# Optimization experiments

Hardware: AMD Instinct MI355X
Metric: run time of the kernel (lower is better)

Reference implementation:

```python
import jax, jax.numpy as jnp
import numpy as np

TWO_N, D = 8192, 256
N = TWO_N // 2


def setup_inputs() -> dict:
    key = jax.random.key(0)
    k1, k2 = jax.random.split(key)
    embeddings = jax.random.normal(k1, (TWO_N, D), dtype=jnp.float32)
    pos_mask = jnp.zeros((N, TWO_N), dtype=bool)  # unused by the loss
    neg_mask = jax.random.randint(k2, (N, TWO_N), 0, 2).astype(bool)
    return {"embeddings": embeddings, "pos_mask": pos_mask, "neg_mask": neg_mask}


def reference(embeddings, pos_mask, neg_mask):
    # d[i, j] = <e_i, e_j>  (other_embeddings defaults to embeddings)
    d = jnp.matmul(embeddings, embeddings.T)            # [2N, 2N]
    n = embeddings.shape[0] // 2
    rows = d[:n]                                        # [N, 2N] (only rows 0..N-1 used)
    ap = rows[jnp.arange(n), jnp.arange(n) + n]         # d[i, i+N], shape [N]
    # masked sum_j exp(d[i,j] - ap_i) over negatives, then log(1 + .)
    expm = jnp.exp(rows - ap[:, None])                  # [N, 2N]
    j_all = jnp.log1p(jnp.sum(jnp.where(neg_mask, expm, 0.0), axis=1))  # [N]
    return jnp.mean(j_all)
```

## Files before the change

### kernel.cpp

```cpp
#include <hip/hip_runtime.h>
#include <math.h>

#define TWO_N 8192
#define NR 4096
#define D 256
#define PMW 128
#define L2E 1.44269504088896340736f

typedef __attribute__((ext_vector_type(8))) short bf16x8;
typedef __attribute__((ext_vector_type(4))) float f32x4;

#define AS1V const __attribute__((address_space(1))) void
#define AS3V __attribute__((address_space(3))) void
#define WAITVM(n) asm volatile("s_waitcnt vmcnt(" #n ")" ::: "memory")

__device__ inline unsigned short f2bf(float x) {
  unsigned u = __builtin_bit_cast(unsigned, x);
  u += 0x7fffu + ((u >> 16) & 1u);
  return (unsigned short)(u >> 16);
}

__global__ __launch_bounds__(256) void prep_kernel(
    const float* __restrict__ emb, const unsigned char* __restrict__ negm,
    unsigned short* __restrict__ ebf, unsigned long long* __restrict__ pm,
    float* __restrict__ apl, double* __restrict__ rowsum) {
  const int b = blockIdx.x, t = threadIdx.x;
  if (b < 1024) {
    const size_t i = ((size_t)b * 256 + t) * 8;
    const float4 a = *reinterpret_cast<const float4*>(emb + i);
    const float4 c = *reinterpret_cast<const float4*>(emb + i + 4);
    union { unsigned short s[8]; bf16x8 v; } o;
    o.s[0] = f2bf(a.x); o.s[1] = f2bf(a.y); o.s[2] = f2bf(a.z); o.s[3] = f2bf(a.w);
    o.s[4] = f2bf(c.x); o.s[5] = f2bf(c.y); o.s[6] = f2bf(c.z); o.s[7] = f2bf(c.w);
    *reinterpret_cast<bf16x8*>(ebf + i) = o.v;
  } else if (b < 3072) {
    const int w = (b - 1024) * 256 + t;
    const uint4* p = reinterpret_cast<const uint4*>(negm + (size_t)w * 64);
    unsigned long long acc = 0;
#pragma unroll
    for (int q = 0; q < 4; ++q) {
      const uint4 v = p[q];
      unsigned bb = 0;
      bb |= (v.x & 1u) | ((v.x >> 7) & 2u) | ((v.x >> 14) & 4u) | ((v.x >> 21) & 8u);
      bb |= ((v.y & 1u) | ((v.y >> 7) & 2u) | ((v.y >> 14) & 4u) | ((v.y >> 21) & 8u)) << 4;
      bb |= ((v.z & 1u) | ((v.z >> 7) & 2u) | ((v.z >> 14) & 4u) | ((v.z >> 21) & 8u)) << 8;
      bb |= ((v.w & 1u) | ((v.w >> 7) & 2u) | ((v.w >> 14) & 4u) | ((v.w >> 21) & 8u)) << 12;
      acc |= (unsigned long long)bb << (q * 16);
    }
    pm[w] = acc;
  } else {
    const int lane = t & 63, wid = t >> 6;
    const int i = (b - 3072) * 4 + wid;
    const float4 a = *reinterpret_cast<const float4*>(emb + (size_t)i * D + lane * 4);
    const float4 c = *reinterpret_cast<const float4*>(emb + (size_t)(i + NR) * D + lane * 4);
    float s = a.x * c.x + a.y * c.y + a.z * c.z + a.w * c.w;
#pragma unroll
    for (int off = 32; off >= 1; off >>= 1) s += __shfl_xor(s, off, 64);
    if (lane == 0) { apl[i] = -s * L2E; rowsum[i] = 0.0; }
  }
}

__global__ __launch_bounds__(512) void fused_mfma(
    const unsigned short* __restrict__ ebf, const unsigned long long* __restrict__ pm,
    const float* __restrict__ apl, double* __restrict__ rowsum) {
  __shared__ unsigned short As[4][128 * 64];
  __shared__ unsigned short Bs[4][128 * 64];
  const int t = threadIdx.x, lane = t & 63, wid = t >> 6;
  const int wr = wid >> 2, wc = wid & 3;
  const int sw = (blockIdx.x & 7) * 32 + (blockIdx.x >> 3);
  const int bi = sw >> 3, chunk = sw & 7;
  const int g = lane >> 4, cl = lane & 15;
  const int srow = lane >> 3;
  const int sc8 = ((lane & 7) ^ srow) * 8;

  float apv[4][4];
#pragma unroll
  for (int m = 0; m < 4; ++m)
#pragma unroll
    for (int r2 = 0; r2 < 4; ++r2)
      apv[m][r2] = apl[bi * 128 + wr * 64 + m * 16 + g * 4 + r2];

#pragma unroll
  for (int kt = 0; kt < 4; ++kt)
#pragma unroll
    for (int q = 0; q < 2; ++q) {
      const int rbase = wid * 16 + q * 8;
      const unsigned short* gp = ebf + (size_t)(bi * 128 + rbase + srow) * D + kt * 64 + sc8;
      __builtin_amdgcn_global_load_lds((AS1V*)gp, (AS3V*)(As[kt] + rbase * 64), 16, 0, 0);
    }

  auto STAGEB = [&](int gk) {
    const int kt = gk & 3, bjj = gk >> 2;
#pragma unroll
    for (int q = 0; q < 2; ++q) {
      const int rbase = wid * 16 + q * 8;
      const unsigned short* gp =
          ebf + (size_t)(chunk * 1024 + bjj * 128 + rbase + srow) * D + kt * 64 + sc8;
      __builtin_amdgcn_global_load_lds((AS1V*)gp, (AS3V*)(Bs[kt] + rbase * 64), 16, 0, 0);
    }
  };
  STAGEB(0); STAGEB(1); STAGEB(2);

  double rs[4][4] = {};

  for (int bj = 0; bj < 8; ++bj) {
    f32x4 acc[4][2] = {};
#pragma unroll
    for (int kt = 0; kt < 4; ++kt) {
      const int gkt = bj * 4 + kt;
      if (kt == 2 && bj == 7) { WAITVM(2); }
      else if (kt == 3 && bj == 7) { WAITVM(0); }
      else { WAITVM(4); }
      __builtin_amdgcn_s_barrier();
      __builtin_amdgcn_sched_barrier(0);
      __builtin_amdgcn_s_setprio(1);
#pragma unroll
      for (int kk = 0; kk < 2; ++kk) {
        const int cswz = ((kk * 4 + g) ^ (lane & 7)) * 8;
        bf16x8 af[4], bf2[2];
#pragma unroll
        for (int m = 0; m < 4; ++m)
          af[m] = *reinterpret_cast<const bf16x8*>(&As[kt][(wr * 64 + m * 16 + cl) * 64 + cswz]);
#pragma unroll
        for (int n = 0; n < 2; ++n)
          bf2[n] = *reinterpret_cast<const bf16x8*>(&Bs[kt][(wc * 32 + n * 16 + cl) * 64 + cswz]);
#pragma unroll
        for (int m = 0; m < 4; ++m)
#pragma unroll
          for (int n = 0; n < 2; ++n)
            acc[m][n] = __builtin_amdgcn_mfma_f32_16x16x32_bf16(af[m], bf2[n], acc[m][n], 0, 0, 0);
      }
      __builtin_amdgcn_s_setprio(0);
      __builtin_amdgcn_s_barrier();
      __builtin_amdgcn_sched_barrier(0);
      if (kt < 3) {
        if (gkt + 3 < 32) STAGEB(gkt + 3);
      }
    }
    unsigned long long mw[4][4];
#pragma unroll
    for (int m = 0; m < 4; ++m)
#pragma unroll
      for (int r2 = 0; r2 < 4; ++r2) {
        const int row = bi * 128 + wr * 64 + m * 16 + g * 4 + r2;
        mw[m][r2] = pm[(size_t)row * PMW + (chunk * 8 + bj) * 2 + (wc >> 1)];
      }
    __builtin_amdgcn_sched_barrier(0);
    if (bj * 4 + 6 < 32) STAGEB(bj * 4 + 6);
#pragma unroll
    for (int m = 0; m < 4; ++m)
#pragma unroll
      for (int r2 = 0; r2 < 4; ++r2) {
#pragma unroll
        for (int n = 0; n < 2; ++n) {
          float tt = fmaf(acc[m][n][r2], L2E, apv[m][r2]);
          tt = fminf(fmaxf(tt, -1020.f), 960.f);
          const float kf = floorf(tt);
          float mant;
          asm("v_exp_f32 %0, %1" : "=v"(mant) : "v"(tt - kf));
          const int bitp = (wc & 1) * 32 + n * 16 + cl;
          mant = ((mw[m][r2] >> bitp) & 1) ? mant : 0.f;
          rs[m][r2] += ldexp((double)mant, (int)kf);
        }
      }
  }

#pragma unroll
  for (int m = 0; m < 4; ++m)
#pragma unroll
    for (int r2 = 0; r2 < 4; ++r2) {
      double v = rs[m][r2];
#pragma unroll
      for (int off = 8; off >= 1; off >>= 1) v += __shfl_xor(v, off, 64);
      if (cl == 0)
        atomicAdd(&rowsum[bi * 128 + wr * 64 + m * 16 + g * 4 + r2], v);
    }
}

__global__ __launch_bounds__(1024) void finalize_kernel(const double* __restrict__ rowsum,
                                                        float* __restrict__ out) {
  __shared__ double red[16];
  const int t = threadIdx.x;
  double s = 0.0;
#pragma unroll
  for (int k = 0; k < 4; ++k) s += log1p(rowsum[t + k * 1024]);
#pragma unroll
  for (int off = 32; off >= 1; off >>= 1) s += __shfl_xor(s, off, 64);
  if ((t & 63) == 0) red[t >> 6] = s;
  __syncthreads();
  if (t == 0) {
    double tot = 0.0;
#pragma unroll
    for (int w = 0; w < 16; ++w) tot += red[w];
    out[0] = (float)(tot * (1.0 / NR));
  }
}

extern "C" void kernel_launch(void* const* d_in, const int* in_sizes, int n_in,
                              void* d_out, int out_size, void* d_ws, size_t ws_size,
                              hipStream_t stream) {
  const float* emb = (const float*)d_in[0];
  const unsigned char* negm = (const unsigned char*)d_in[2];
  float* out = (float*)d_out;
  char* ws = (char*)d_ws;
  unsigned short* ebf = (unsigned short*)ws;
  unsigned long long* pm = (unsigned long long*)(ws + (1u << 22));
  float* apl = (float*)(ws + (2u << 22));
  double* rowsum = (double*)(ws + (2u << 22) + 16384);

  prep_kernel<<<dim3(4096), dim3(256), 0, stream>>>(emb, negm, ebf, pm, apl, rowsum);
  fused_mfma<<<dim3(256), dim3(512), 0, stream>>>(ebf, pm, apl, rowsum);
  finalize_kernel<<<dim3(1), dim3(1024), 0, stream>>>(rowsum, out);
}
```

Baseline: 273.7 us.

## Widen B tile to 256 columns with double-buffered staging and cheaper exp scaling

The fused GEMM+exp kernel now processes 256 B columns per step with 4x4 MFMA accumulators per wave instead of 4x2. It double-buffers B K-slices instead of triple-buffering, and moves the mask word loads inside the last K step. The ldexp on a double is replaced with a constructed power-of-two double multiply, and the A-row log-offsets are loaded as float4. This aims to raise A-fragment reuse and cut exp-scaling cost, at the price of more accumulator registers and possibly lower occupancy.

```diff
diff --git a/kernel.cpp b/kernel.cpp
--- a/kernel.cpp
+++ b/kernel.cpp
@@ -18,6 +18,16 @@
   unsigned u = __builtin_bit_cast(unsigned, x);
   u += 0x7fffu + ((u >> 16) & 1u);
   return (unsigned short)(u >> 16);
+}
+
+__device__ inline float exp2_hw(float x) {
+#if __has_builtin(__builtin_amdgcn_exp2f)
+  return __builtin_amdgcn_exp2f(x);
+#else
+  float r;
+  asm("v_exp_f32 %0, %1" : "=v"(r) : "v"(x));
+  return r;
+#endif
 }
 
 __global__ __launch_bounds__(256) void prep_kernel(
@@ -64,7 +74,7 @@
     const unsigned short* __restrict__ ebf, const unsigned long long* __restrict__ pm,
     const float* __restrict__ apl, double* __restrict__ rowsum) {
   __shared__ unsigned short As[4][128 * 64];
-  __shared__ unsigned short Bs[4][128 * 64];
+  __shared__ unsigned short Bs[2][256 * 64];
   const int t = threadIdx.x, lane = t & 63, wid = t >> 6;
   const int wr = wid >> 2, wc = wid & 3;
   const int sw = (blockIdx.x & 7) * 32 + (blockIdx.x >> 3);
@@ -75,10 +85,10 @@
 
   float apv[4][4];
 #pragma unroll
-  for (int m = 0; m < 4; ++m)
-#pragma unroll
-    for (int r2 = 0; r2 < 4; ++r2)
-      apv[m][r2] = apl[bi * 128 + wr * 64 + m * 16 + g * 4 + r2];
+  for (int m = 0; m < 4; ++m) {
+    const float4 v = *reinterpret_cast<const float4*>(apl + bi * 128 + wr * 64 + m * 16 + g * 4);
+    apv[m][0] = v.x; apv[m][1] = v.y; apv[m][2] = v.z; apv[m][3] = v.w;
+  }
 
 #pragma unroll
   for (int kt = 0; kt < 4; ++kt)
@@ -92,24 +102,24 @@
   auto STAGEB = [&](int gk) {
     const int kt = gk & 3, bjj = gk >> 2;
 #pragma unroll
-    for (int q = 0; q < 2; ++q) {
-      const int rbase = wid * 16 + q * 8;
+    for (int q = 0; q < 4; ++q) {
+      const int rbase = wid * 32 + q * 8;
       const unsigned short* gp =
-          ebf + (size_t)(chunk * 1024 + bjj * 128 + rbase + srow) * D + kt * 64 + sc8;
-      __builtin_amdgcn_global_load_lds((AS1V*)gp, (AS3V*)(Bs[kt] + rbase * 64), 16, 0, 0);
+          ebf + (size_t)(chunk * 1024 + bjj * 256 + rbase + srow) * D + kt * 64 + sc8;
+      __builtin_amdgcn_global_load_lds((AS1V*)gp, (AS3V*)(Bs[gk & 1] + rbase * 64), 16, 0, 0);
     }
   };
-  STAGEB(0); STAGEB(1); STAGEB(2);
+  STAGEB(0); STAGEB(1);
 
   double rs[4][4] = {};
 
-  for (int bj = 0; bj < 8; ++bj) {
-    f32x4 acc[4][2] = {};
+  for (int bj = 0; bj < 4; ++bj) {
+    f32x4 acc[4][4] = {};
+    unsigned long long mw[4][4];
 #pragma unroll
     for (int kt = 0; kt < 4; ++kt) {
       const int gkt = bj * 4 + kt;
-      if (kt == 2 && bj == 7) { WAITVM(2); }
-      else if (kt == 3 && bj == 7) { WAITVM(0); }
+      if (kt == 3) { if (bj == 3) { WAITVM(0); } else { WAITVM(4); } }
       else { WAITVM(4); }
       __builtin_amdgcn_s_barrier();
       __builtin_amdgcn_sched_barrier(0);
@@ -117,52 +127,49 @@
 #pragma unroll
       for (int kk = 0; kk < 2; ++kk) {
         const int cswz = ((kk * 4 + g) ^ (lane & 7)) * 8;
-        bf16x8 af[4], bf2[2];
+        bf16x8 af[4], bf[4];
 #pragma unroll
         for (int m = 0; m < 4; ++m)
           af[m] = *reinterpret_cast<const bf16x8*>(&As[kt][(wr * 64 + m * 16 + cl) * 64 + cswz]);
 #pragma unroll
-        for (int n = 0; n < 2; ++n)
-          bf2[n] = *reinterpret_cast<const bf16x8*>(&Bs[kt][(wc * 32 + n * 16 + cl) * 64 + cswz]);
+        for (int n = 0; n < 4; ++n)
+          bf[n] = *reinterpret_cast<const bf16x8*>(&Bs[gkt & 1][(wc * 64 + n * 16 + cl) * 64 + cswz]);
 #pragma unroll
         for (int m = 0; m < 4; ++m)
 #pragma unroll
-          for (int n = 0; n < 2; ++n)
-            acc[m][n] = __builtin_amdgcn_mfma_f32_16x16x32_bf16(af[m], bf2[n], acc[m][n], 0, 0, 0);
+          for (int n = 0; n < 4; ++n)
+            acc[m][n] = __builtin_amdgcn_mfma_f32_16x16x32_bf16(af[m], bf[n], acc[m][n], 0, 0, 0);
       }
       __builtin_amdgcn_s_setprio(0);
       __builtin_amdgcn_s_barrier();
       __builtin_amdgcn_sched_barrier(0);
-      if (kt < 3) {
-        if (gkt + 3 < 32) STAGEB(gkt + 3);
+      if (kt == 3) {
+#pragma unroll
+        for (int m = 0; m < 4; ++m)
+#pragma unroll
+          for (int r2 = 0; r2 < 4; ++r2) {
+            const int row = bi * 128 + wr * 64 + m * 16 + g * 4 + r2;
+            mw[m][r2] = pm[(size_t)row * PMW + chunk * 16 + bj * 4 + wc];
+          }
+        __builtin_amdgcn_sched_barrier(0);
       }
-    }
-    unsigned long long mw[4][4];
+      if (gkt + 2 < 16) STAGEB(gkt + 2);
+      __builtin_amdgcn_sched_barrier(0);
+    }
 #pragma unroll
     for (int m = 0; m < 4; ++m)
 #pragma unroll
-      for (int r2 = 0; r2 < 4; ++r2) {
-        const int row = bi * 128 + wr * 64 + m * 16 + g * 4 + r2;
-        mw[m][r2] = pm[(size_t)row * PMW + (chunk * 8 + bj) * 2 + (wc >> 1)];
-      }
-    __builtin_amdgcn_sched_barrier(0);
-    if (bj * 4 + 6 < 32) STAGEB(bj * 4 + 6);
-#pragma unroll
-    for (int m = 0; m < 4; ++m)
-#pragma unroll
-      for (int r2 = 0; r2 < 4; ++r2) {
-#pragma unroll
-        for (int n = 0; n < 2; ++n) {
+      for (int n = 0; n < 4; ++n)
+#pragma unroll
+        for (int r2 = 0; r2 < 4; ++r2) {
           float tt = fmaf(acc[m][n][r2], L2E, apv[m][r2]);
-          tt = fminf(fmaxf(tt, -1020.f), 960.f);
+          tt = fminf(fmaxf(tt, -1020.f), 1000.f);
           const float kf = floorf(tt);
-          float mant;
-          asm("v_exp_f32 %0, %1" : "=v"(mant) : "v"(tt - kf));
-          const int bitp = (wc & 1) * 32 + n * 16 + cl;
-          mant = ((mw[m][r2] >> bitp) & 1) ? mant : 0.f;
-          rs[m][r2] += ldexp((double)mant, (int)kf);
+          const float mant = exp2_hw(tt - kf);
+          const float mm = ((mw[m][r2] >> (n * 16 + cl)) & 1) ? mant : 0.f;
+          const long long ebits = (long long)(1023 + (int)kf) << 52;
+          rs[m][r2] += (double)mm * __builtin_bit_cast(double, ebits);
         }
-      }
   }
 
 #pragma unroll
@@ -172,8 +179,7 @@
       double v = rs[m][r2];
 #pragma unroll
       for (int off = 8; off >= 1; off >>= 1) v += __shfl_xor(v, off, 64);
-      if (cl == 0)
-        atomicAdd(&rowsum[bi * 128 + wr * 64 + m * 16 + g * 4 + r2], v);
+      if (cl == 0) atomicAdd(&rowsum[bi * 128 + wr * 64 + m * 16 + g * 4 + r2], v);
     }
 }
 
```

Result: faster. 267.3 us (-2.3%).
